# Kernel optimization log

Measured on AMD Instinct MI355X. Metric: run time of the kernel, lower is better.

## Reference

```python
import jax, jax.numpy as jnp
import numpy as np

NUM_Q = 10000
DK = 128   # dim_key (width of each memory slot and of embeddings)
DV = 64    # dim_value (number of memory slots)
B = 128
S = 200


def setup_inputs() -> dict:
    key = jax.random.key(0)
    ks = jax.random.split(key, 16)
    sc = 0.05
    return {
        "question_seq": jax.random.randint(ks[0], (B, S), 0, NUM_Q),
        "correct_seq": jax.random.randint(ks[1], (B, S), 0, 2),
        "k_emb": jax.random.normal(ks[2], (NUM_Q, DK), jnp.float32) * sc,
        "v_emb": jax.random.normal(ks[3], (2 * NUM_Q, DK), jnp.float32) * sc,
        "Mk": jax.random.normal(ks[4], (DV, DK), jnp.float32) * sc,
        "Mv0": jax.random.normal(ks[5], (DV, DK), jnp.float32) * sc,
        "fW": jax.random.normal(ks[6], (2 * DK, DK), jnp.float32) * sc,
        "fb": jnp.zeros((DK,), jnp.float32),
        "eW": jax.random.normal(ks[7], (DK, DK), jnp.float32) * sc,
        "eb": jnp.zeros((DK,), jnp.float32),
        "aW": jax.random.normal(ks[8], (DK, DK), jnp.float32) * sc,
        "ab": jnp.zeros((DK,), jnp.float32),
        "pW": jax.random.normal(ks[9], (DK, 1), jnp.float32) * sc,
        "pb": jnp.zeros((1,), jnp.float32),
    }


def reference(question_seq, correct_seq, k_emb, v_emb, Mk, Mv0, fW, fb, eW, eb, aW, ab, pW, pb):
    num_q = k_emb.shape[0]
    x = question_seq + num_q * correct_seq            # [B,S]
    k = k_emb[question_seq]                           # [B,S,DK]
    v = v_emb[x]                                      # [B,S,DK]

    w = jax.nn.softmax(jnp.einsum('bsk,vk->bsv', k, Mk), axis=-1)  # [B,S,DV]
    e = jax.nn.sigmoid(v @ eW + eb)                   # [B,S,DK]
    a = jnp.tanh(v @ aW + ab)                         # [B,S,DK]

    Mvt0 = jnp.broadcast_to(Mv0[None], (question_seq.shape[0],) + Mv0.shape)  # [B,DV,DK]

    def step(Mvt, inp):
        wt, et, at = inp                              # [B,DV],[B,DK],[B,DK]
        read = jnp.einsum('bv,bvk->bk', wt, Mvt)      # read BEFORE update (Mv[:, :-1])
        we = wt[:, :, None] * et[:, None, :]          # [B,DV,DK]
        wa = wt[:, :, None] * at[:, None, :]
        Mvt_new = Mvt * (1.0 - we) + wa
        return Mvt_new, read

    xs = (w.transpose(1, 0, 2), e.transpose(1, 0, 2), a.transpose(1, 0, 2))
    _, reads = jax.lax.scan(step, Mvt0, xs)           # reads: [S,B,DK]
    reads = reads.transpose(1, 0, 2)                  # [B,S,DK]

    f = jnp.tanh(jnp.concatenate([reads, k], axis=-1) @ fW + fb)  # [B,S,DK]
    # dropout is identity in eval mode
    predict_score = jax.nn.sigmoid(f @ pW + pb).squeeze(-1)       # [B,S]
    return predict_score
```

## Files before the change

kernel.cpp:

```cpp
#include <hip/hip_runtime.h>
#include <math.h>


typedef float f32x4 __attribute__((ext_vector_type(4)));
typedef short bf16x8 __attribute__((ext_vector_type(8)));

__device__ __forceinline__ float sigm(float x) { return 1.0f / (1.0f + __expf(-x)); }
__device__ __forceinline__ short f2bf(float x) {
    union { float f; unsigned u; } v; v.f = x;
    return (short)((v.u + 0x7FFFu + ((v.u >> 16) & 1u)) >> 16);
}

__global__ __launch_bounds__(256) void prep_kernel(
    const float* __restrict__ eW, const float* __restrict__ aW,
    const float* __restrict__ fW, const float* __restrict__ Mk,
    short* __restrict__ eWt, short* __restrict__ aWt,
    short* __restrict__ fWrt, short* __restrict__ fWkt,
    short* __restrict__ Mkb)
{
    const int t = threadIdx.x;
    if (blockIdx.x == 4) {
        for (int idx = t; idx < 1024; idx += 256) {
            const int row = idx >> 4, c8 = idx & 15;
            const float4 f0 = *(const float4*)(Mk + row * 128 + c8 * 8);
            const float4 f1 = *(const float4*)(Mk + row * 128 + c8 * 8 + 4);
            bf16x8 v;
            v[0] = f2bf(f0.x); v[1] = f2bf(f0.y); v[2] = f2bf(f0.z); v[3] = f2bf(f0.w);
            v[4] = f2bf(f1.x); v[5] = f2bf(f1.y); v[6] = f2bf(f1.z); v[7] = f2bf(f1.w);
            *(bf16x8*)(Mkb + row * 128 + c8 * 8) = v;
        }
        return;
    }
    const float* src; short* dst;
    switch (blockIdx.x) {
        case 0:  src = eW;             dst = eWt;  break;
        case 1:  src = aW;             dst = aWt;  break;
        case 2:  src = fW;             dst = fWrt; break;
        default: src = fW + 128 * 128; dst = fWkt; break;
    }
    const int n  = t & 127;
    const int kh = (t >> 7) * 64;
    for (int k0 = kh; k0 < kh + 64; k0 += 8) {
        bf16x8 v;
        #pragma unroll
        for (int kk = 0; kk < 8; ++kk) v[kk] = f2bf(src[(k0 + kk) * 128 + n]);
        *(bf16x8*)(dst + n * 128 + k0) = v;
    }
}

__global__ __launch_bounds__(256) void veakf_kernel(
    const float* __restrict__ v_emb, const float* __restrict__ k_emb,
    const short* __restrict__ eWt, const short* __restrict__ aWt,
    const short* __restrict__ fWkt, const short* __restrict__ Mkb,
    const float* __restrict__ eb, const float* __restrict__ ab,
    const float* __restrict__ fb,
    int num_q, int nbe,
    float* __restrict__ e_all, float* __restrict__ a_all,
    float* __restrict__ kf_all, float* __restrict__ w_all)
{
    __shared__ __align__(16) short Bsh[128 * 128];
    const int t = threadIdx.x;
    const bool ea = ((int)blockIdx.x < nbe);
    const int nrows = ea ? 2 * num_q : num_q;
    const int R0 = (ea ? (int)blockIdx.x : (int)blockIdx.x - nbe) * 64;
    const float* Asrc = ea ? v_emb : k_emb;

    const int wv = t >> 6;
    const int lr = t & 15;
    const int lk = (t & 63) >> 4;
    const int arow = wv * 16 + lr;
    int gr = R0 + arow; if (gr > nrows - 1) gr = nrows - 1;

    float4 a0[4], a1[4];
    #pragma unroll
    for (int ks = 0; ks < 4; ++ks) {
        const int off = (ks * 4 + lk) * 8;
        a0[ks] = *(const float4*)(Asrc + (size_t)gr * 128 + off);
        a1[ks] = *(const float4*)(Asrc + (size_t)gr * 128 + off + 4);
    }
    {
        const short* B1 = ea ? eWt : fWkt;
        #pragma unroll
        for (int i = 0; i < 8; ++i) {
            const int c = t + 256 * i;
            const int row = c >> 4, ch = c & 15;
            *(bf16x8*)&Bsh[row * 128 + ((ch ^ (row & 7)) * 8)] =
                *(const bf16x8*)(B1 + row * 128 + ch * 8);
        }
    }
    bf16x8 af[4];
    #pragma unroll
    for (int ks = 0; ks < 4; ++ks) {
        bf16x8 v;
        v[0] = f2bf(a0[ks].x); v[1] = f2bf(a0[ks].y);
        v[2] = f2bf(a0[ks].z); v[3] = f2bf(a0[ks].w);
        v[4] = f2bf(a1[ks].x); v[5] = f2bf(a1[ks].y);
        v[6] = f2bf(a1[ks].z); v[7] = f2bf(a1[ks].w);
        af[ks] = v;
    }
    __syncthreads();

    f32x4 acc[8];
    #pragma unroll
    for (int ct = 0; ct < 8; ++ct) acc[ct] = (f32x4)0.f;
    #pragma unroll
    for (int ks = 0; ks < 4; ++ks) {
        const int chunk = ks * 4 + lk;
        #pragma unroll
        for (int ct = 0; ct < 8; ++ct) {
            const int n = ct * 16 + lr;
            const bf16x8 b = *(const bf16x8*)&Bsh[n * 128 + ((chunk ^ (n & 7)) * 8)];
            acc[ct] = __builtin_amdgcn_mfma_f32_16x16x32_bf16(af[ks], b, acc[ct], 0, 0, 0);
        }
    }
    if (ea) {
        #pragma unroll
        for (int ct = 0; ct < 8; ++ct) {
            const int col = ct * 16 + lr;
            const float ebv = eb[col];
            #pragma unroll
            for (int r = 0; r < 4; ++r) {
                const int row = R0 + wv * 16 + lk * 4 + r;
                if (row < nrows)
                    e_all[(size_t)row * 128 + col] = sigm(acc[ct][r] + ebv);
            }
        }
    } else {
        #pragma unroll
        for (int ct = 0; ct < 8; ++ct) {
            const int col = ct * 16 + lr;
            const float fbv = fb[col];
            #pragma unroll
            for (int r = 0; r < 4; ++r) {
                const int row = R0 + wv * 16 + lk * 4 + r;
                if (row < nrows)
                    kf_all[(size_t)row * 128 + col] = acc[ct][r] + fbv;
            }
        }
    }
    __syncthreads();

    if (ea) {
        #pragma unroll
        for (int i = 0; i < 8; ++i) {
            const int c = t + 256 * i;
            const int row = c >> 4, ch = c & 15;
            *(bf16x8*)&Bsh[row * 128 + ((ch ^ (row & 7)) * 8)] =
                *(const bf16x8*)(aWt + row * 128 + ch * 8);
        }
    } else {
        #pragma unroll
        for (int i = 0; i < 4; ++i) {
            const int c = t + 256 * i;
            const int row = c >> 4, ch = c & 15;
            *(bf16x8*)&Bsh[row * 128 + ((ch ^ (row & 7)) * 8)] =
                *(const bf16x8*)(Mkb + row * 128 + ch * 8);
        }
    }
    __syncthreads();

    if (ea) {
        #pragma unroll
        for (int ct = 0; ct < 8; ++ct) acc[ct] = (f32x4)0.f;
        #pragma unroll
        for (int ks = 0; ks < 4; ++ks) {
            const int chunk = ks * 4 + lk;
            #pragma unroll
            for (int ct = 0; ct < 8; ++ct) {
                const int n = ct * 16 + lr;
                const bf16x8 b = *(const bf16x8*)&Bsh[n * 128 + ((chunk ^ (n & 7)) * 8)];
                acc[ct] = __builtin_amdgcn_mfma_f32_16x16x32_bf16(af[ks], b, acc[ct], 0, 0, 0);
            }
        }
        #pragma unroll
        for (int ct = 0; ct < 8; ++ct) {
            const int col = ct * 16 + lr;
            const float abv = ab[col];
            #pragma unroll
            for (int r = 0; r < 4; ++r) {
                const int row = R0 + wv * 16 + lk * 4 + r;
                if (row < nrows)
                    a_all[(size_t)row * 128 + col] = tanhf(acc[ct][r] + abv);
            }
        }
    } else {
        f32x4 accw[4];
        #pragma unroll
        for (int ct = 0; ct < 4; ++ct) accw[ct] = (f32x4)0.f;
        #pragma unroll
        for (int ks = 0; ks < 4; ++ks) {
            const int chunk = ks * 4 + lk;
            #pragma unroll
            for (int ct = 0; ct < 4; ++ct) {
                const int n = ct * 16 + lr;
                const bf16x8 b = *(const bf16x8*)&Bsh[n * 128 + ((chunk ^ (n & 7)) * 8)];
                accw[ct] = __builtin_amdgcn_mfma_f32_16x16x32_bf16(af[ks], b, accw[ct], 0, 0, 0);
            }
        }
        #pragma unroll
        for (int r = 0; r < 4; ++r) {
            const float x0 = accw[0][r], x1 = accw[1][r];
            const float x2 = accw[2][r], x3 = accw[3][r];
            float m = fmaxf(fmaxf(x0, x1), fmaxf(x2, x3));
            #pragma unroll
            for (int mk = 1; mk < 16; mk <<= 1) m = fmaxf(m, __shfl_xor(m, mk));
            const float e0 = __expf(x0 - m), e1 = __expf(x1 - m);
            const float e2 = __expf(x2 - m), e3 = __expf(x3 - m);
            float s = (e0 + e1) + (e2 + e3);
            #pragma unroll
            for (int mk = 1; mk < 16; mk <<= 1) s += __shfl_xor(s, mk);
            const float inv = 1.0f / s;
            const int row = R0 + wv * 16 + lk * 4 + r;
            if (row < nrows) {
                float* wr = w_all + (size_t)row * 64 + lr;
                wr[0]  = e0 * inv; wr[16] = e1 * inv;
                wr[32] = e2 * inv; wr[48] = e3 * inv;
            }
        }
    }
}

__global__ __launch_bounds__(256) void scan_kernel(
    const float* __restrict__ Mv0,
    const int* __restrict__ qseq, const int* __restrict__ cseq,
    const float* __restrict__ w_all, const float* __restrict__ e_all,
    const float* __restrict__ a_all, int num_q,
    unsigned short* __restrict__ reads_bf)
{
    const int t  = threadIdx.x;
    const int j  = t & 31;
    const int vg = t >> 5;
    const int cq = blockIdx.x & 3;
    const int b  = blockIdx.x >> 2;
    const int jg = cq * 32 + j;

    float Mv[8];
    #pragma unroll
    for (int i = 0; i < 8; ++i) Mv[i] = Mv0[(vg * 8 + i) * 128 + jg];

    __shared__ float wb[2][8][64];
    __shared__ float ebuf[2][8][32];
    __shared__ float abuf[2][8][32];
    __shared__ float part[2][8][8][32];
    __shared__ int sq[200], sx[200];

    if (t < 200) {
        const int q = qseq[b * 200 + t];
        const int c = cseq[b * 200 + t];
        sq[t] = q * 16;
        sx[t] = (q + num_q * c) * 32 + cq * 8;
    }
    __syncthreads();

    const float4* w4 = (const float4*)w_all;
    const float4* e4 = (const float4*)e_all;
    const float4* a4 = (const float4*)a_all;

    float4 rg;
    if (t < 128)      { rg = w4[sq[t >> 4] + (t & 15)];                       ((float4*)wb[0])[t] = rg; }
    else if (t < 192) { const int u = t - 128; rg = e4[sx[u >> 3] + (u & 7)]; ((float4*)ebuf[0])[u] = rg; }
    else              { const int u = t - 192; rg = a4[sx[u >> 3] + (u & 7)]; ((float4*)abuf[0])[u] = rg; }
    __syncthreads();

    int cb = 0, pbuf = 0;
    for (int c = 0; c < 25; ++c) {
        if (c < 24) {
            const int s0 = (c + 1) * 8;
            if (t < 128)      rg = w4[sq[s0 + (t >> 4)] + (t & 15)];
            else if (t < 192) { const int u = t - 128; rg = e4[sx[s0 + (u >> 3)] + (u & 7)]; }
            else              { const int u = t - 192; rg = a4[sx[s0 + (u >> 3)] + (u & 7)]; }
        }
        #pragma unroll
        for (int st = 0; st < 8; ++st) {
            const float e_j = ebuf[cb][st][j];
            const float a_j = abuf[cb][st][j];
            const float* wrow = &wb[cb][st][vg * 8];
            float r0 = 0.f, r1 = 0.f, r2 = 0.f, r3 = 0.f;
            #pragma unroll
            for (int v4i = 0; v4i < 2; ++v4i) {
                const float4 w4v = *(const float4*)&wrow[v4i * 4];
                const int v = v4i * 4;
                r0 = fmaf(w4v.x, Mv[v + 0], r0);
                Mv[v + 0] = fmaf(w4v.x, fmaf(-Mv[v + 0], e_j, a_j), Mv[v + 0]);
                r1 = fmaf(w4v.y, Mv[v + 1], r1);
                Mv[v + 1] = fmaf(w4v.y, fmaf(-Mv[v + 1], e_j, a_j), Mv[v + 1]);
                r2 = fmaf(w4v.z, Mv[v + 2], r2);
                Mv[v + 2] = fmaf(w4v.z, fmaf(-Mv[v + 2], e_j, a_j), Mv[v + 2]);
                r3 = fmaf(w4v.w, Mv[v + 3], r3);
                Mv[v + 3] = fmaf(w4v.w, fmaf(-Mv[v + 3], e_j, a_j), Mv[v + 3]);
            }
            part[pbuf][st][vg][j] = (r0 + r1) + (r2 + r3);
        }
        if (c < 24) {
            if (t < 128)      ((float4*)wb[cb ^ 1])[t] = rg;
            else if (t < 192) ((float4*)ebuf[cb ^ 1])[t - 128] = rg;
            else              ((float4*)abuf[cb ^ 1])[t - 192] = rg;
        }
        __syncthreads();
        {
            const int st = t >> 5, jr = t & 31;
            const float* pp = &part[pbuf][st][0][jr];
            float r = 0.f;
            #pragma unroll
            for (int g = 0; g < 8; ++g) r += pp[g * 32];
            reads_bf[(size_t)b * 200 * 128 + (size_t)(c * 8 + st) * 128 + cq * 32 + jr]
                = (unsigned short)f2bf(r);
        }
        cb ^= 1; pbuf ^= 1;
    }
}

__global__ __launch_bounds__(256) void out_kernel(
    const int* __restrict__ qseq,
    const unsigned short* __restrict__ reads_bf,
    const short* __restrict__ fWrt, const float* __restrict__ kf_all,
    const float* __restrict__ pW, const float* __restrict__ pb,
    int ntok, float* __restrict__ out)
{
    __shared__ __align__(16) short Ash[64 * 128];
    __shared__ int qi[64];
    const int t = threadIdx.x;
    const int R0 = blockIdx.x * 64;
    if (t < 64) { int r = R0 + t; qi[t] = qseq[r < ntok ? r : ntok - 1]; }
    #pragma unroll
    for (int i = 0; i < 4; ++i) {
        const int c = t + 256 * i;
        const int row = c >> 4, ch = c & 15;
        int gr = R0 + row; if (gr > ntok - 1) gr = ntok - 1;
        const bf16x8 v = *(const bf16x8*)(reads_bf + (size_t)gr * 128 + ch * 8);
        *(bf16x8*)&Ash[row * 128 + ((ch ^ (row & 7)) * 8)] = v;
    }
    __syncthreads();

    const int wv = t >> 6;
    const int lr = t & 15;
    const int lk = (t & 63) >> 4;
    const int arow = wv * 16 + lr;

    f32x4 acc[8];
    #pragma unroll
    for (int ct = 0; ct < 8; ++ct) {
        const int col = ct * 16 + lr;
        #pragma unroll
        for (int r = 0; r < 4; ++r) {
            const int q = qi[wv * 16 + lk * 4 + r];
            acc[ct][r] = kf_all[(size_t)q * 128 + col];
        }
    }
    #pragma unroll
    for (int ks = 0; ks < 4; ++ks) {
        const int chunk = ks * 4 + lk;
        const bf16x8 af = *(const bf16x8*)&Ash[arow * 128 + ((chunk ^ (arow & 7)) * 8)];
        const int kb = ks * 32 + lk * 8;
        #pragma unroll
        for (int ct = 0; ct < 8; ++ct) {
            const int n = ct * 16 + lr;
            const bf16x8 bfr = *(const bf16x8*)(fWrt + n * 128 + kb);
            acc[ct] = __builtin_amdgcn_mfma_f32_16x16x32_bf16(af, bfr, acc[ct], 0, 0, 0);
        }
    }
    const float pb0 = pb[0];
    float s0 = 0.f, s1 = 0.f, s2 = 0.f, s3 = 0.f;
    #pragma unroll
    for (int ct = 0; ct < 8; ++ct) {
        const float pw = pW[ct * 16 + lr];
        s0 = fmaf(tanhf(acc[ct][0]), pw, s0);
        s1 = fmaf(tanhf(acc[ct][1]), pw, s1);
        s2 = fmaf(tanhf(acc[ct][2]), pw, s2);
        s3 = fmaf(tanhf(acc[ct][3]), pw, s3);
    }
    #pragma unroll
    for (int off = 1; off < 16; off <<= 1) {
        s0 += __shfl_xor(s0, off);
        s1 += __shfl_xor(s1, off);
        s2 += __shfl_xor(s2, off);
        s3 += __shfl_xor(s3, off);
    }
    if (lr == 0) {
        const int row = R0 + wv * 16 + lk * 4;
        if (row + 0 < ntok) out[row + 0] = sigm(s0 + pb0);
        if (row + 1 < ntok) out[row + 1] = sigm(s1 + pb0);
        if (row + 2 < ntok) out[row + 2] = sigm(s2 + pb0);
        if (row + 3 < ntok) out[row + 3] = sigm(s3 + pb0);
    }
}

extern "C" void kernel_launch(void* const* d_in, const int* in_sizes, int n_in,
                              void* d_out, int out_size, void* d_ws, size_t ws_size,
                              hipStream_t stream)
{
    const int*   qseq  = (const int*)d_in[0];
    const int*   cseq  = (const int*)d_in[1];
    const float* k_emb = (const float*)d_in[2];
    const float* v_emb = (const float*)d_in[3];
    const float* Mk    = (const float*)d_in[4];
    const float* Mv0   = (const float*)d_in[5];
    const float* fW    = (const float*)d_in[6];
    const float* fb    = (const float*)d_in[7];
    const float* eW    = (const float*)d_in[8];
    const float* eb    = (const float*)d_in[9];
    const float* aW    = (const float*)d_in[10];
    const float* ab    = (const float*)d_in[11];
    const float* pW    = (const float*)d_in[12];
    const float* pb    = (const float*)d_in[13];

    const int num_q = in_sizes[2] / 128;
    const int ntok  = in_sizes[0];
    const int Bb    = ntok / 200;
    const int NV    = 2 * num_q;

    float* ws = (float*)d_ws;
    float* w_all  = ws;
    float* e_all  = w_all  + (size_t)num_q * 64;
    float* a_all  = e_all  + (size_t)NV * 128;
    float* kf_all = a_all  + (size_t)NV * 128;
    short* eWt    = (short*)(kf_all + (size_t)num_q * 128);
    short* aWt    = eWt  + 128 * 128;
    short* fWrt   = aWt  + 128 * 128;
    short* fWkt   = fWrt + 128 * 128;
    short* Mkb    = fWkt + 128 * 128;
    unsigned short* reads_bf = (unsigned short*)(Mkb + 64 * 128);

    prep_kernel<<<5, 256, 0, stream>>>(eW, aW, fW, Mk, eWt, aWt, fWrt, fWkt, Mkb);
    const int nbe = (NV + 63) / 64, nbk = (num_q + 63) / 64;
    veakf_kernel<<<nbe + nbk, 256, 0, stream>>>(v_emb, k_emb, eWt, aWt, fWkt, Mkb,
                                                eb, ab, fb, num_q, nbe,
                                                e_all, a_all, kf_all, w_all);
    scan_kernel<<<Bb * 4, 256, 0, stream>>>(Mv0, qseq, cseq, w_all, e_all, a_all,
                                            num_q, reads_bf);
    out_kernel<<<(ntok + 63) / 64, 256, 0, stream>>>(qseq, reads_bf, fWrt, kf_all,
                                                     pW, pb, ntok, (float*)d_out);
}
```

Before: 69.46 us.

## Split fused embedding GEMM blocks per output type and use fast exp-based tanh

The embedding-table projection kernel now launches one block per (output type, row tile) instead of each block computing two GEMMs back to back. This doubles the grid, removes a mid-kernel barrier and weight reload, and lets the GPU spread the work more evenly. The cost is that each 64-row tile of A is now loaded and converted to bf16 twice. tanhf is also replaced by a clamped __expf-based tanh in the a-projection and the output kernel, trading a little accuracy for cheaper transcendental evaluation.

```diff
diff --git a/kernel.cpp b/kernel.cpp
--- a/kernel.cpp
+++ b/kernel.cpp
@@ -6,6 +6,11 @@
 typedef short bf16x8 __attribute__((ext_vector_type(8)));
 
 __device__ __forceinline__ float sigm(float x) { return 1.0f / (1.0f + __expf(-x)); }
+__device__ __forceinline__ float ftanh(float x) {
+    x = fminf(20.f, fmaxf(-20.f, x));
+    const float t = __expf(2.0f * x);
+    return (t - 1.0f) / (t + 1.0f);
+}
 __device__ __forceinline__ short f2bf(float x) {
     union { float f; unsigned u; } v; v.f = x;
     return (short)((v.u + 0x7FFFu + ((v.u >> 16) & 1u)) >> 16);
@@ -54,15 +59,20 @@
     const short* __restrict__ fWkt, const short* __restrict__ Mkb,
     const float* __restrict__ eb, const float* __restrict__ ab,
     const float* __restrict__ fb,
-    int num_q, int nbe,
+    int num_q, int nbe, int nbk,
     float* __restrict__ e_all, float* __restrict__ a_all,
     float* __restrict__ kf_all, float* __restrict__ w_all)
 {
     __shared__ __align__(16) short Bsh[128 * 128];
     const int t = threadIdx.x;
-    const bool ea = ((int)blockIdx.x < nbe);
+    const int bid = blockIdx.x;
+    int type, R0;
+    if (bid < nbe)                { type = 0; R0 = bid * 64; }
+    else if (bid < 2 * nbe)       { type = 1; R0 = (bid - nbe) * 64; }
+    else if (bid < 2 * nbe + nbk) { type = 2; R0 = (bid - 2 * nbe) * 64; }
+    else                          { type = 3; R0 = (bid - 2 * nbe - nbk) * 64; }
+    const bool ea = (type < 2);
     const int nrows = ea ? 2 * num_q : num_q;
-    const int R0 = (ea ? (int)blockIdx.x : (int)blockIdx.x - nbe) * 64;
     const float* Asrc = ea ? v_emb : k_emb;
 
     const int wv = t >> 6;
@@ -79,13 +89,14 @@
         a1[ks] = *(const float4*)(Asrc + (size_t)gr * 128 + off + 4);
     }
     {
-        const short* B1 = ea ? eWt : fWkt;
-        #pragma unroll
-        for (int i = 0; i < 8; ++i) {
+        const short* Bt = (type == 0) ? eWt : (type == 1) ? aWt
+                        : (type == 2) ? fWkt : Mkb;
+        const int niter = (type == 3) ? 4 : 8;
+        for (int i = 0; i < niter; ++i) {
             const int c = t + 256 * i;
             const int row = c >> 4, ch = c & 15;
             *(bf16x8*)&Bsh[row * 128 + ((ch ^ (row & 7)) * 8)] =
-                *(const bf16x8*)(B1 + row * 128 + ch * 8);
+                *(const bf16x8*)(Bt + row * 128 + ch * 8);
         }
     }
     bf16x8 af[4];
@@ -100,90 +111,7 @@
     }
     __syncthreads();
 
-    f32x4 acc[8];
-    #pragma unroll
-    for (int ct = 0; ct < 8; ++ct) acc[ct] = (f32x4)0.f;
-    #pragma unroll
-    for (int ks = 0; ks < 4; ++ks) {
-        const int chunk = ks * 4 + lk;
-        #pragma unroll
-        for (int ct = 0; ct < 8; ++ct) {
-            const int n = ct * 16 + lr;
-            const bf16x8 b = *(const bf16x8*)&Bsh[n * 128 + ((chunk ^ (n & 7)) * 8)];
-            acc[ct] = __builtin_amdgcn_mfma_f32_16x16x32_bf16(af[ks], b, acc[ct], 0, 0, 0);
-        }
-    }
-    if (ea) {
-        #pragma unroll
-        for (int ct = 0; ct < 8; ++ct) {
-            const int col = ct * 16 + lr;
-            const float ebv = eb[col];
-            #pragma unroll
-            for (int r = 0; r < 4; ++r) {
-                const int row = R0 + wv * 16 + lk * 4 + r;
-                if (row < nrows)
-                    e_all[(size_t)row * 128 + col] = sigm(acc[ct][r] + ebv);
-            }
-        }
-    } else {
-        #pragma unroll
-        for (int ct = 0; ct < 8; ++ct) {
-            const int col = ct * 16 + lr;
-            const float fbv = fb[col];
-            #pragma unroll
-            for (int r = 0; r < 4; ++r) {
-                const int row = R0 + wv * 16 + lk * 4 + r;
-                if (row < nrows)
-                    kf_all[(size_t)row * 128 + col] = acc[ct][r] + fbv;
-            }
-        }
-    }
-    __syncthreads();
-
-    if (ea) {
-        #pragma unroll
-        for (int i = 0; i < 8; ++i) {
-            const int c = t + 256 * i;
-            const int row = c >> 4, ch = c & 15;
-            *(bf16x8*)&Bsh[row * 128 + ((ch ^ (row & 7)) * 8)] =
-                *(const bf16x8*)(aWt + row * 128 + ch * 8);
-        }
-    } else {
-        #pragma unroll
-        for (int i = 0; i < 4; ++i) {
-            const int c = t + 256 * i;
-            const int row = c >> 4, ch = c & 15;
-            *(bf16x8*)&Bsh[row * 128 + ((ch ^ (row & 7)) * 8)] =
-                *(const bf16x8*)(Mkb + row * 128 + ch * 8);
-        }
-    }
-    __syncthreads();
-
-    if (ea) {
-        #pragma unroll
-        for (int ct = 0; ct < 8; ++ct) acc[ct] = (f32x4)0.f;
-        #pragma unroll
-        for (int ks = 0; ks < 4; ++ks) {
-            const int chunk = ks * 4 + lk;
-            #pragma unroll
-            for (int ct = 0; ct < 8; ++ct) {
-                const int n = ct * 16 + lr;
-                const bf16x8 b = *(const bf16x8*)&Bsh[n * 128 + ((chunk ^ (n & 7)) * 8)];
-                acc[ct] = __builtin_amdgcn_mfma_f32_16x16x32_bf16(af[ks], b, acc[ct], 0, 0, 0);
-            }
-        }
-        #pragma unroll
-        for (int ct = 0; ct < 8; ++ct) {
-            const int col = ct * 16 + lr;
-            const float abv = ab[col];
-            #pragma unroll
-            for (int r = 0; r < 4; ++r) {
-                const int row = R0 + wv * 16 + lk * 4 + r;
-                if (row < nrows)
-                    a_all[(size_t)row * 128 + col] = tanhf(acc[ct][r] + abv);
-            }
-        }
-    } else {
+    if (type == 3) {
         f32x4 accw[4];
         #pragma unroll
         for (int ct = 0; ct < 4; ++ct) accw[ct] = (f32x4)0.f;
@@ -215,6 +143,37 @@
                 float* wr = w_all + (size_t)row * 64 + lr;
                 wr[0]  = e0 * inv; wr[16] = e1 * inv;
                 wr[32] = e2 * inv; wr[48] = e3 * inv;
+            }
+        }
+        return;
+    }
+
+    f32x4 acc[8];
+    #pragma unroll
+    for (int ct = 0; ct < 8; ++ct) acc[ct] = (f32x4)0.f;
+    #pragma unroll
+    for (int ks = 0; ks < 4; ++ks) {
+        const int chunk = ks * 4 + lk;
+        #pragma unroll
+        for (int ct = 0; ct < 8; ++ct) {
+            const int n = ct * 16 + lr;
+            const bf16x8 b = *(const bf16x8*)&Bsh[n * 128 + ((chunk ^ (n & 7)) * 8)];
+            acc[ct] = __builtin_amdgcn_mfma_f32_16x16x32_bf16(af[ks], b, acc[ct], 0, 0, 0);
+        }
+    }
+    #pragma unroll
+    for (int ct = 0; ct < 8; ++ct) {
+        const int col = ct * 16 + lr;
+        #pragma unroll
+        for (int r = 0; r < 4; ++r) {
+            const int row = R0 + wv * 16 + lk * 4 + r;
+            if (row < nrows) {
+                if (type == 0)
+                    e_all[(size_t)row * 128 + col]  = sigm(acc[ct][r] + eb[col]);
+                else if (type == 1)
+                    a_all[(size_t)row * 128 + col]  = ftanh(acc[ct][r] + ab[col]);
+                else
+                    kf_all[(size_t)row * 128 + col] = acc[ct][r] + fb[col];
             }
         }
     }
@@ -364,10 +323,10 @@
     #pragma unroll
     for (int ct = 0; ct < 8; ++ct) {
         const float pw = pW[ct * 16 + lr];
-        s0 = fmaf(tanhf(acc[ct][0]), pw, s0);
-        s1 = fmaf(tanhf(acc[ct][1]), pw, s1);
-        s2 = fmaf(tanhf(acc[ct][2]), pw, s2);
-        s3 = fmaf(tanhf(acc[ct][3]), pw, s3);
+        s0 = fmaf(ftanh(acc[ct][0]), pw, s0);
+        s1 = fmaf(ftanh(acc[ct][1]), pw, s1);
+        s2 = fmaf(ftanh(acc[ct][2]), pw, s2);
+        s3 = fmaf(ftanh(acc[ct][3]), pw, s3);
     }
     #pragma unroll
     for (int off = 1; off < 16; off <<= 1) {
@@ -423,9 +382,9 @@
 
     prep_kernel<<<5, 256, 0, stream>>>(eW, aW, fW, Mk, eWt, aWt, fWrt, fWkt, Mkb);
     const int nbe = (NV + 63) / 64, nbk = (num_q + 63) / 64;
-    veakf_kernel<<<nbe + nbk, 256, 0, stream>>>(v_emb, k_emb, eWt, aWt, fWkt, Mkb,
-                                                eb, ab, fb, num_q, nbe,
-                                                e_all, a_all, kf_all, w_all);
+    veakf_kernel<<<2 * nbe + 2 * nbk, 256, 0, stream>>>(
+        v_emb, k_emb, eWt, aWt, fWkt, Mkb, eb, ab, fb, num_q, nbe, nbk,
+        e_all, a_all, kf_all, w_all);
     scan_kernel<<<Bb * 4, 256, 0, stream>>>(Mv0, qseq, cseq, w_all, e_all, a_all,
                                             num_q, reads_bf);
     out_kernel<<<(ntok + 63) / 64, 256, 0, stream>>>(qseq, reads_bf, fWrt, kf_all,
```

Result: slower. 72.63 us (+4.6%).
